# Performance work log

Measured on AMD Instinct MI355X. Metric: run time of the kernel, lower is better.

## Reference

```python
import jax, jax.numpy as jnp
import numpy as np

K, D = 1024, 256


def setup_inputs() -> dict:
    key = jax.random.key(0)
    k1, k2 = jax.random.split(key)
    z_e = jax.random.normal(k1, (32, D, 32, 32), dtype=jnp.float32)
    # torch init: uniform_(-1/K, 1/K)
    emb_weight = jax.random.uniform(k2, (K, D), minval=-1.0 / K, maxval=1.0 / K, dtype=jnp.float32)
    return {"z_e": z_e, "emb_weight": emb_weight}


def reference(z_e, emb_weight):
    B, C, W, H = z_e.shape
    # [B, W, H, C] -> flatten to [N, C]
    z = jnp.transpose(z_e, (0, 2, 3, 1))
    z_flat = z.reshape(-1, C)
    # squared euclidean distances; argmin is identical to argmin of cdist
    d2 = (
        jnp.sum(z_flat * z_flat, axis=1, keepdims=True)
        - 2.0 * (z_flat @ emb_weight.T)
        + jnp.sum(emb_weight * emb_weight, axis=1)
    )  # [N, K]
    indices = jnp.argmin(d2, axis=1)  # [N]
    z_q = emb_weight[indices].reshape(B, W, H, C)
    # straight-through: forward value equals z_q, gradient passes to z_e
    z_q_st = z + jax.lax.stop_gradient(z_q - z)
    z_q_out = jnp.transpose(z_q, (0, 3, 1, 2))
    z_q_st_out = jnp.transpose(z_q_st, (0, 3, 1, 2))
    return (z_q_st_out, z_q_out, indices.reshape(B, W * H))
```

## Files before the change

### kernel.cpp

```cpp
#include <hip/hip_runtime.h>
#include <cfloat>
#include <cstdint>

#define THRESH 1.25e-4f

typedef __attribute__((ext_vector_type(8))) _Float16 half8;
typedef __attribute__((ext_vector_type(8))) unsigned short upk8;
typedef __attribute__((ext_vector_type(4))) float facc4;

__device__ __forceinline__ unsigned short f2h(float x) {
  _Float16 h = (_Float16)x;
  return __builtin_bit_cast(unsigned short, h);
}


__global__ __launch_bounds__(256) void precompute_kernel(
    const float* __restrict__ emb, float* __restrict__ Csq,
    unsigned short* __restrict__ ehT, int* __restrict__ flagCount) {
  int blk = blockIdx.x, t = threadIdx.x;
  if (blk < 4) {
    int k = blk * 256 + t;
    const float4* e4 = (const float4*)(emb + ((size_t)k << 8));
    double acc = 0.0;
    for (int d4 = 0; d4 < 64; ++d4) {
      float4 e = e4[d4];
      acc += (double)(e.x * e.x) + (double)(e.y * e.y) +
             (double)(e.z * e.z) + (double)(e.w * e.w);
    }
    Csq[k] = (float)acc;
    if (blk == 0 && t == 0) *flagCount = 0;
  } else {
    int linear = (blk - 4) * 256 + t;
    int code = linear & 1023, kg = linear >> 10;
    const float* ep = emb + ((size_t)code << 8) + (kg << 3);
    float4 e0 = *(const float4*)ep;
    float4 e1 = *(const float4*)(ep + 4);
    upk8 pk;
    pk[0] = f2h(e0.x); pk[1] = f2h(e0.y); pk[2] = f2h(e0.z); pk[3] = f2h(e0.w);
    pk[4] = f2h(e1.x); pk[5] = f2h(e1.y); pk[6] = f2h(e1.z); pk[7] = f2h(e1.w);
    *(upk8*)(ehT + ((size_t)linear << 3)) = pk;
  }
}

__device__ __forceinline__ void stage_half(
    const unsigned short* __restrict__ ehT, char* buf, int h, int t) {
  int w6 = t & 0x1C0;
#pragma unroll
  for (int i = 0; i < 8; ++i) {
    int slot = (i << 9) + t;
    int kg = slot >> 7, cl = slot & 127;
    const unsigned short* g = ehT + (((size_t)(kg << 10) + (h << 7) + cl) << 3);
    char* lp = buf + (((i << 9) + w6) << 4);
    __builtin_amdgcn_global_load_lds(
        (const __attribute__((address_space(1))) unsigned int*)g,
        (__attribute__((address_space(3))) unsigned int*)lp, 16, 0, 0);
  }
}

__global__ __launch_bounds__(512) __attribute__((amdgpu_waves_per_eu(2, 2)))
void phase1_kernel(
    const float* __restrict__ z, const unsigned short* __restrict__ ehT,
    const float* __restrict__ Csq, float* __restrict__ A,
    int* __restrict__ idxbuf, int* __restrict__ flagCount,
    int* __restrict__ flagList) {
  __shared__ char bufA[65536] __attribute__((aligned(16)));
  __shared__ char bufB[65536] __attribute__((aligned(16)));
  __shared__ float Cs[1024];
  __shared__ float mm1[2][4][32], mm2[2][4][32];
  __shared__ int mbi[2][4][32];

  int t = threadIdx.x;
  int n0 = blockIdx.x << 7;
  int b = n0 >> 10, wh0 = n0 & 1023;
  int w = t >> 6, l = t & 63;
  int wv = w & 3, wn = w >> 2;
  int lx = l & 15, lg = l >> 4;

  stage_half(ehT, bufA, 0, t);
  stage_half(ehT, bufB, 1, t);
  ((float2*)Cs)[t] = ((const float2*)Csq)[t];

  half8 afr[2][8];
  double nacc[2] = {0.0, 0.0};
  const float* zb = z + (((size_t)(b * 256)) << 10) + wh0 + wv * 32 + lx;
#pragma unroll
  for (int mi = 0; mi < 2; ++mi) {
#pragma unroll
    for (int kk = 0; kk < 8; ++kk) {
      upk8 pk;
#pragma unroll
      for (int j = 0; j < 8; ++j) {
        int c = kk * 32 + lg * 8 + j;
        float x = zb[((size_t)c << 10) + mi * 16];
        nacc[mi] += (double)(x * x);
        pk[j] = f2h(-2.0f * x);
      }
      afr[mi][kk] = __builtin_bit_cast(half8, pk);
    }
  }
#pragma unroll
  for (int mi = 0; mi < 2; ++mi) {
    double s = nacc[mi];
    s += __shfl_xor(s, 16);
    s += __shfl_xor(s, 32);
    if (wn == 0 && lg == 0) A[n0 + wv * 32 + mi * 16 + lx] = (float)s;
  }
  __syncthreads();

  float m1[8], m2[8];
  int bi[8];
#pragma unroll
  for (int s8 = 0; s8 < 8; ++s8) { m1[s8] = FLT_MAX; m2[s8] = FLT_MAX; bi[s8] = 0; }

#pragma unroll 1
  for (int h = 0; h < 8; ++h) {
    const char* buf = (h & 1) ? bufB : bufA;
    facc4 acc[2][4];
#pragma unroll
    for (int mi = 0; mi < 2; ++mi)
#pragma unroll
      for (int nj = 0; nj < 4; ++nj) {
        facc4 zf = {0.0f, 0.0f, 0.0f, 0.0f};
        acc[mi][nj] = zf;
      }
#pragma unroll
    for (int kk = 0; kk < 8; ++kk) {
      const char* base = buf + (((((kk << 2) + lg) << 7) + (wn << 6) + lx) << 4);
#pragma unroll
      for (int nj = 0; nj < 4; ++nj) {
        half8 bv = *(const half8*)(base + (nj << 8));
        acc[0][nj] = __builtin_amdgcn_mfma_f32_16x16x32_f16(afr[0][kk], bv, acc[0][nj], 0, 0, 0);
        acc[1][nj] = __builtin_amdgcn_mfma_f32_16x16x32_f16(afr[1][kk], bv, acc[1][nj], 0, 0, 0);
      }
    }
    int cbase = (h << 7) + (wn << 6);
#pragma unroll
    for (int nj = 0; nj < 4; ++nj) {
      float csv = Cs[cbase + nj * 16 + lx];
      int code = cbase + nj * 16 + lx;
#pragma unroll
      for (int mi = 0; mi < 2; ++mi)
#pragma unroll
        for (int reg = 0; reg < 4; ++reg) {
          int s8 = mi * 4 + reg;
          float sv = acc[mi][nj][reg] + csv;
          float hi = fmaxf(sv, m1[s8]);
          bool lt = sv < m1[s8];
          m1[s8] = lt ? sv : m1[s8];
          bi[s8] = lt ? code : bi[s8];
          m2[s8] = fminf(m2[s8], hi);
        }
    }
    if (h < 7) {
      asm volatile("s_waitcnt lgkmcnt(0)" ::: "memory");
      __builtin_amdgcn_s_barrier();
      if (h < 6) {
        stage_half(ehT, (h & 1) ? bufB : bufA, h + 2, t);
        asm volatile("s_waitcnt vmcnt(8)" ::: "memory");
      } else {
        asm volatile("s_waitcnt vmcnt(0)" ::: "memory");
      }
      __builtin_amdgcn_s_barrier();
    }
  }

#pragma unroll
  for (int s8 = 0; s8 < 8; ++s8) {
    float M1 = m1[s8], M2 = m2[s8];
    int BI = bi[s8];
    for (int off = 8; off > 0; off >>= 1) {
      float om1 = __shfl_xor(M1, off, 16);
      float om2 = __shfl_xor(M2, off, 16);
      int obi = __shfl_xor(BI, off, 16);
      float lo = fminf(M2, om2);
      bool take = (om1 < M1) || (om1 == M1 && obi < BI);
      float loser = take ? M1 : om1;
      M2 = fminf(lo, loser);
      if (take) { M1 = om1; BI = obi; }
    }
    if (lx == 0) {
      int row = ((s8 >> 2) << 4) + (lg << 2) + (s8 & 3);
      mm1[wn][wv][row] = M1; mm2[wn][wv][row] = M2; mbi[wn][wv][row] = BI;
    }
  }
  __syncthreads();
  if (wn == 0 && lx == 0) {
#pragma unroll
    for (int s8 = 0; s8 < 8; ++s8) {
      int row = ((s8 >> 2) << 4) + (lg << 2) + (s8 & 3);
      float a1v = mm1[0][wv][row], a2v = mm2[0][wv][row];
      int ab = mbi[0][wv][row];
      float b1v = mm1[1][wv][row], b2v = mm2[1][wv][row];
      int bb = mbi[1][wv][row];
      bool tb = (b1v < a1v) || (b1v == a1v && bb < ab);
      float M1 = tb ? b1v : a1v;
      int BI = tb ? bb : ab;
      float M2 = fminf(fminf(a2v, b2v), tb ? a1v : b1v);
      int n = n0 + wv * 32 + row;
      idxbuf[n] = BI;
      if (M2 - M1 < THRESH) {
        int pos = atomicAdd(flagCount, 1);
        flagList[pos] = n;
      }
    }
  }
}

__global__ __launch_bounds__(256) void phase2_kernel(
    const float* __restrict__ z, const float* __restrict__ emb,
    const float* __restrict__ Csq, const float* __restrict__ A,
    int* __restrict__ idxbuf, const int* __restrict__ flagCount,
    const int* __restrict__ flagList) {
  __shared__ float zq[4][260];
  __shared__ float Anv[4];
  __shared__ int nn[4];
  __shared__ float sq[4][4];
  __shared__ int sk[4][4];
  int t = threadIdx.x;
  int w = t >> 6, l = t & 63;
  int cnt = *flagCount;
  int nit = (cnt + 3) >> 2;
  for (int it = blockIdx.x; it < nit; it += gridDim.x) {
    __syncthreads();
    int base = it << 2;
    int mcnt = min(4, cnt - base);
    if (t < 4) {
      if (t < mcnt) { int n = flagList[base + t]; nn[t] = n; Anv[t] = A[n]; }
      else nn[t] = -1;
    }
    __syncthreads();
#pragma unroll
    for (int v = 0; v < 4; ++v) {
      int n = nn[v];
      if (n >= 0) {
        int bb = n >> 10, wh = n & 1023;
        zq[v][t] = z[(((size_t)(bb * 256 + t)) << 10) + wh];
      }
    }
    __syncthreads();

    float dot[4][4];
#pragma unroll
    for (int r = 0; r < 4; ++r)
#pragma unroll
      for (int v = 0; v < 4; ++v) dot[r][v] = 0.0f;

    const float4* e0 = (const float4*)(emb + ((size_t)(t + 0) << 8));
    const float4* e1 = (const float4*)(emb + ((size_t)(t + 256) << 8));
    const float4* e2 = (const float4*)(emb + ((size_t)(t + 512) << 8));
    const float4* e3 = (const float4*)(emb + ((size_t)(t + 768) << 8));
#pragma unroll 8
    for (int d4 = 0; d4 < 64; ++d4) {
      float4 ea = e0[d4], eb = e1[d4], ec = e2[d4], ed = e3[d4];
#pragma unroll
      for (int v = 0; v < 4; ++v) {
        float4 zv = *(const float4*)&zq[v][d4 * 4];
        dot[0][v] += zv.x * ea.x + zv.y * ea.y + zv.z * ea.z + zv.w * ea.w;
        dot[1][v] += zv.x * eb.x + zv.y * eb.y + zv.z * eb.z + zv.w * eb.w;
        dot[2][v] += zv.x * ec.x + zv.y * ec.y + zv.z * ec.z + zv.w * ec.w;
        dot[3][v] += zv.x * ed.x + zv.y * ed.y + zv.z * ed.z + zv.w * ed.w;
      }
    }

    float bq[4];
    int bk[4];
#pragma unroll
    for (int v = 0; v < 4; ++v) { bq[v] = FLT_MAX; bk[v] = 0; }
#pragma unroll
    for (int r = 0; r < 4; ++r) {
      int k = t + (r << 8);
      float Ck = Csq[k];
#pragma unroll
      for (int v = 0; v < 4; ++v) {
        float qv = (Anv[v] - 2.0f * dot[r][v]) + Ck;
        if (qv < bq[v]) { bq[v] = qv; bk[v] = k; }
      }
    }

#pragma unroll
    for (int v = 0; v < 4; ++v) {
      float q = bq[v];
      int kk = bk[v];
      for (int off = 32; off > 0; off >>= 1) {
        float oq = __shfl_xor(q, off);
        int ok = __shfl_xor(kk, off);
        if (oq < q || (oq == q && ok < kk)) { q = oq; kk = ok; }
      }
      if (l == 0) { sq[v][w] = q; sk[v][w] = kk; }
    }
    __syncthreads();
    if (t < mcnt) {
      float q = sq[t][0];
      int kk = sk[t][0];
#pragma unroll
      for (int j = 1; j < 4; ++j) {
        float oq = sq[t][j];
        int ok = sk[t][j];
        if (oq < q || (oq == q && ok < kk)) { q = oq; kk = ok; }
      }
      idxbuf[nn[t]] = kk;
    }
  }
}

__global__ __launch_bounds__(256) void gather_kernel(
    const float* __restrict__ emb, const int* __restrict__ idxbuf,
    float* __restrict__ out) {
  __shared__ int sidx[32];
  __shared__ float se[256][36];
  int tid = threadIdx.x;
  int blk = blockIdx.x;
  int n0 = blk * 32;
  int b = n0 >> 10, wh0 = n0 & 1023;
  float* out0 = out;
  float* out1 = out + 8388608;
  float* out2 = out + 16777216;
  if (tid < 32) {
    int ix = idxbuf[n0 + tid];
    sidx[tid] = ix;
    out2[n0 + tid] = (float)ix;
  }
  __syncthreads();
  {
    int v = tid >> 3, d8 = tid & 7;
    int row = sidx[v];
    const float4* e4 = (const float4*)(emb + ((size_t)row << 8));
    for (int it = 0; it < 8; ++it) {
      int d4 = it * 8 + d8;
      float4 e = e4[d4];
      se[d4 * 4 + 0][v] = e.x; se[d4 * 4 + 1][v] = e.y;
      se[d4 * 4 + 2][v] = e.z; se[d4 * 4 + 3][v] = e.w;
    }
  }
  __syncthreads();
  {
    int slot = tid & 7, crow = tid >> 3;
#pragma unroll
    for (int it = 0; it < 8; ++it) {
      int c = it * 32 + crow;
      float4 val = *(const float4*)&se[c][slot * 4];
      size_t o = (((size_t)(b * 256 + c)) << 10) + wh0 + slot * 4;
      *(float4*)(out0 + o) = val;
      *(float4*)(out1 + o) = val;
    }
  }
}

extern "C" void kernel_launch(void* const* d_in, const int* in_sizes, int n_in,
                              void* d_out, int out_size, void* d_ws, size_t ws_size,
                              hipStream_t stream) {
  const float* z = (const float*)d_in[0];
  const float* emb = (const float*)d_in[1];
  float* ws = (float*)d_ws;
  float* Csq = ws;
  float* A = ws + 1024;
  int* idxbuf = (int*)(ws + 33792);
  int* flagCount = (int*)(ws + 66560);
  int* flagList = (int*)(ws + 66576);
  unsigned short* ehT = (unsigned short*)(ws + 99344);

  precompute_kernel<<<132, 256, 0, stream>>>(emb, Csq, ehT, flagCount);
  phase1_kernel<<<256, 512, 0, stream>>>(z, ehT, Csq, A, idxbuf, flagCount, flagList);
  phase2_kernel<<<1024, 256, 0, stream>>>(z, emb, Csq, A, idxbuf, flagCount, flagList);
  gather_kernel<<<1024, 256, 0, stream>>>(emb, idxbuf, (float*)d_out);
}
```

Measured before the change: 102.4 us.

## Fuse codebook gather and output writes into phase1, patch flagged rows in phase2

The separate gather kernel is removed. Phase1 now writes its argmin indices to shared memory, gathers the chosen codebook rows into the reused LDS staging buffer, and writes the transposed z_q outputs and the indices directly. Phase2 overwrites the output columns only for the rows it re-checks. This saves a kernel launch and the round trip through the index buffer, but phase1 now carries extra gather and store work, and phase2 writes strided scattered columns.

```diff
diff --git a/kernel.cpp b/kernel.cpp
--- a/kernel.cpp
+++ b/kernel.cpp
@@ -60,14 +60,16 @@
 __global__ __launch_bounds__(512) __attribute__((amdgpu_waves_per_eu(2, 2)))
 void phase1_kernel(
     const float* __restrict__ z, const unsigned short* __restrict__ ehT,
-    const float* __restrict__ Csq, float* __restrict__ A,
-    int* __restrict__ idxbuf, int* __restrict__ flagCount,
-    int* __restrict__ flagList) {
-  __shared__ char bufA[65536] __attribute__((aligned(16)));
-  __shared__ char bufB[65536] __attribute__((aligned(16)));
+    const float* __restrict__ Csq, const float* __restrict__ emb,
+    float* __restrict__ A, float* __restrict__ out,
+    int* __restrict__ flagCount, int* __restrict__ flagList) {
+  __shared__ char lds[135168] __attribute__((aligned(16)));
   __shared__ float Cs[1024];
   __shared__ float mm1[2][4][32], mm2[2][4][32];
   __shared__ int mbi[2][4][32];
+  __shared__ int fidx[128];
+  char* bufA = lds;
+  char* bufB = lds + 65536;
 
   int t = threadIdx.x;
   int n0 = blockIdx.x << 7;
@@ -196,12 +198,48 @@
       float M1 = tb ? b1v : a1v;
       int BI = tb ? bb : ab;
       float M2 = fminf(fminf(a2v, b2v), tb ? a1v : b1v);
-      int n = n0 + wv * 32 + row;
-      idxbuf[n] = BI;
+      int rowi = wv * 32 + row;
+      fidx[rowi] = BI;
       if (M2 - M1 < THRESH) {
         int pos = atomicAdd(flagCount, 1);
-        flagList[pos] = n;
-      }
+        flagList[pos] = n0 + rowi;
+      }
+    }
+  }
+  __syncthreads();
+
+  float* out2 = out + 16777216;
+  if (t < 128) out2[n0 + t] = (float)fidx[t];
+  float* se = (float*)lds;
+  {
+    int v = t >> 3, d8 = t & 7;
+#pragma unroll 1
+    for (int pass = 0; pass < 2; ++pass) {
+      int vv = pass * 64 + v;
+      const float4* e4 = (const float4*)(emb + ((size_t)fidx[vv] << 8));
+#pragma unroll
+      for (int it = 0; it < 8; ++it) {
+        int d4 = it * 8 + d8;
+        float4 e = e4[d4];
+        se[(d4 * 4 + 0) * 132 + vv] = e.x;
+        se[(d4 * 4 + 1) * 132 + vv] = e.y;
+        se[(d4 * 4 + 2) * 132 + vv] = e.z;
+        se[(d4 * 4 + 3) * 132 + vv] = e.w;
+      }
+    }
+  }
+  __syncthreads();
+  {
+    float* out0 = out;
+    float* out1 = out + 8388608;
+    int slot = t & 31, crow = t >> 5;
+#pragma unroll 1
+    for (int it = 0; it < 16; ++it) {
+      int c = it * 16 + crow;
+      float4 val = *(const float4*)&se[c * 132 + slot * 4];
+      size_t o = (((size_t)(b * 256 + c)) << 10) + wh0 + slot * 4;
+      *(float4*)(out0 + o) = val;
+      *(float4*)(out1 + o) = val;
     }
   }
 }
@@ -209,13 +247,14 @@
 __global__ __launch_bounds__(256) void phase2_kernel(
     const float* __restrict__ z, const float* __restrict__ emb,
     const float* __restrict__ Csq, const float* __restrict__ A,
-    int* __restrict__ idxbuf, const int* __restrict__ flagCount,
+    float* __restrict__ out, const int* __restrict__ flagCount,
     const int* __restrict__ flagList) {
   __shared__ float zq[4][260];
   __shared__ float Anv[4];
   __shared__ int nn[4];
   __shared__ float sq[4][4];
   __shared__ int sk[4][4];
+  __shared__ int skk[4];
   int t = threadIdx.x;
   int w = t >> 6, l = t & 63;
   int cnt = *flagCount;
@@ -298,50 +337,18 @@
         int ok = sk[t][j];
         if (oq < q || (oq == q && ok < kk)) { q = oq; kk = ok; }
       }
-      idxbuf[nn[t]] = kk;
-    }
-  }
-}
-
-__global__ __launch_bounds__(256) void gather_kernel(
-    const float* __restrict__ emb, const int* __restrict__ idxbuf,
-    float* __restrict__ out) {
-  __shared__ int sidx[32];
-  __shared__ float se[256][36];
-  int tid = threadIdx.x;
-  int blk = blockIdx.x;
-  int n0 = blk * 32;
-  int b = n0 >> 10, wh0 = n0 & 1023;
-  float* out0 = out;
-  float* out1 = out + 8388608;
-  float* out2 = out + 16777216;
-  if (tid < 32) {
-    int ix = idxbuf[n0 + tid];
-    sidx[tid] = ix;
-    out2[n0 + tid] = (float)ix;
-  }
-  __syncthreads();
-  {
-    int v = tid >> 3, d8 = tid & 7;
-    int row = sidx[v];
-    const float4* e4 = (const float4*)(emb + ((size_t)row << 8));
-    for (int it = 0; it < 8; ++it) {
-      int d4 = it * 8 + d8;
-      float4 e = e4[d4];
-      se[d4 * 4 + 0][v] = e.x; se[d4 * 4 + 1][v] = e.y;
-      se[d4 * 4 + 2][v] = e.z; se[d4 * 4 + 3][v] = e.w;
-    }
-  }
-  __syncthreads();
-  {
-    int slot = tid & 7, crow = tid >> 3;
-#pragma unroll
-    for (int it = 0; it < 8; ++it) {
-      int c = it * 32 + crow;
-      float4 val = *(const float4*)&se[c][slot * 4];
-      size_t o = (((size_t)(b * 256 + c)) << 10) + wh0 + slot * 4;
-      *(float4*)(out0 + o) = val;
-      *(float4*)(out1 + o) = val;
+      skk[t] = kk;
+    }
+    __syncthreads();
+    for (int v = 0; v < mcnt; ++v) {
+      int n = nn[v];
+      int kk2 = skk[v];
+      int bb = n >> 10, wh = n & 1023;
+      float val = emb[((size_t)kk2 << 8) + t];
+      size_t o = (((size_t)(bb * 256 + t)) << 10) + wh;
+      out[o] = val;
+      out[8388608 + o] = val;
+      if (t == 0) out[16777216 + n] = (float)kk2;
     }
   }
 }
@@ -354,13 +361,13 @@
   float* ws = (float*)d_ws;
   float* Csq = ws;
   float* A = ws + 1024;
-  int* idxbuf = (int*)(ws + 33792);
   int* flagCount = (int*)(ws + 66560);
   int* flagList = (int*)(ws + 66576);
   unsigned short* ehT = (unsigned short*)(ws + 99344);
 
   precompute_kernel<<<132, 256, 0, stream>>>(emb, Csq, ehT, flagCount);
-  phase1_kernel<<<256, 512, 0, stream>>>(z, ehT, Csq, A, idxbuf, flagCount, flagList);
-  phase2_kernel<<<1024, 256, 0, stream>>>(z, emb, Csq, A, idxbuf, flagCount, flagList);
-  gather_kernel<<<1024, 256, 0, stream>>>(emb, idxbuf, (float*)d_out);
-}
+  phase1_kernel<<<256, 512, 0, stream>>>(z, ehT, Csq, emb, A, (float*)d_out,
+                                         flagCount, flagList);
+  phase2_kernel<<<1024, 256, 0, stream>>>(z, emb, Csq, A, (float*)d_out,
+                                          flagCount, flagList);
+}
```

Result: no change. 104.0 us (+1.6%).
